# Optimization experiments

Measured on AMD Instinct MI355X. Metric: run time of the kernel, lower is better.

The kernel has to match this reference:

```python
import jax, jax.numpy as jnp
import numpy as np

B, T, P, C = 1, 256, 88, 128   # batch, time frames, 88 piano pitches, hidden_per_pitch
HEADS, WIN, NLAYERS = 4, 25, 2
HD = C // HEADS


def setup_inputs() -> dict:
    ks = jax.random.split(jax.random.key(0), 8)
    s = 0.02
    return {
        "x": jax.random.normal(ks[0], (B, T, P, C), jnp.float32),
        "condition": jax.random.normal(ks[1], (B, T, P, 2), jnp.float32),
        "mask": jax.random.uniform(ks[2], (B, T, P), jnp.float32),
        # fusion linear: Linear(hidden_per_pitch + 3, hidden_per_pitch)
        "linear_w": jax.random.normal(ks[3], (C, C + 3), jnp.float32) * s,
        "linear_b": jnp.zeros((C,), jnp.float32),
        # shared NeighborhoodAttention2D params (nn.Sequential repeats the same module)
        "qkv_w": jax.random.normal(ks[4], (3 * C, C), jnp.float32) * s,
        "qkv_b": jnp.zeros((3 * C,), jnp.float32),
        "rpb": jax.random.normal(ks[5], (HEADS, 2 * WIN - 1, 2 * WIN - 1), jnp.float32) * s,
        "proj_w": jax.random.normal(ks[6], (C, C), jnp.float32) * s,
        "proj_b": jnp.zeros((C,), jnp.float32),
    }


def _nbr_idx(n, w):
    # NATTEN edge-clamped windows: window start is clamped so every query sees w keys.
    start = jnp.clip(jnp.arange(n) - (w - 1) // 2, 0, n - w)
    idx = start[:, None] + jnp.arange(w)             # [n, w] absolute key indices
    rel = idx - jnp.arange(n)[:, None] + (w - 1)     # [n, w] rpb indices in [0, 2w-2]
    return idx, rel


def na2d(x, qkv_w, qkv_b, rpb, proj_w, proj_b):
    b, h, w_, c = x.shape
    qkv = (x @ qkv_w.T + qkv_b).reshape(b, h, w_, 3, HEADS, HD)
    q, k, v = (jnp.moveaxis(qkv[..., i, :, :], 3, 1) for i in range(3))  # [b,heads,h,w,hd]
    q = q * (HD ** -0.5)

    idx_h, rel_h = _nbr_idx(h, WIN)
    idx_w, rel_w = _nbr_idx(w_, WIN)

    def score_step(_, ki):
        kg = k[:, :, idx_h[:, ki]][:, :, :, idx_w]
        s = jnp.einsum('bhijd,bhijkd->bhijk', q, kg)
        s = s + rpb[:, rel_h[:, ki]][:, :, rel_w][None]
        return None, s

    _, scores = jax.lax.scan(score_step, None, jnp.arange(WIN))
    scores = jnp.moveaxis(scores, 0, 4)
    attn = jax.nn.softmax(scores.reshape(b, HEADS, h, w_, WIN * WIN), axis=-1)
    attn = attn.reshape(b, HEADS, h, w_, WIN, WIN)

    def out_step(acc, ki):
        vg = v[:, :, idx_h[:, ki]][:, :, :, idx_w]
        return acc + jnp.einsum('bhijk,bhijkd->bhijd', attn[..., ki, :], vg), None

    out, _ = jax.lax.scan(out_step, jnp.zeros_like(q), jnp.arange(WIN))
    out = jnp.moveaxis(out, 1, 3).reshape(b, h, w_, c)      # merge heads
    return out @ proj_w.T + proj_b


def reference(x, condition, mask, linear_w, linear_b, qkv_w, qkv_b, rpb, proj_w, proj_b):
    cat = jnp.concatenate([x, condition, mask[..., None]], axis=-1)  # [B,T,P,C+3]
    y = jax.nn.relu(cat @ linear_w.T + linear_b)
    for _ in range(NLAYERS):  # same module repeated -> shared weights
        y = na2d(y, qkv_w, qkv_b, rpb, proj_w, proj_b)
    return y
```

## Files before the change

### kernel.cpp

```cpp
#include <hip/hip_runtime.h>
#include <hip/hip_fp16.h>

#define TT 256
#define PP 88
#define CC 128
#define NN (TT * PP)
#define HEADS 4
#define HD 32
#define WIN 25
#define RPBW 49
#define RPBSZ (RPBW * RPBW)
#define SCALE 0.17677669529663687f
#define LOG2E 1.4426950408889634f
#define QSC (SCALE * LOG2E)

#define KVROW 11264
#define KVAARWS 258

#if __has_builtin(__builtin_amdgcn_exp2f)
#define EXP2(x) __builtin_amdgcn_exp2f(x)
#else
#define EXP2(x) exp2f(x)
#endif

typedef _Float16 f16;
typedef f16 f16x8 __attribute__((ext_vector_type(8)));
typedef f16 f16x8u __attribute__((ext_vector_type(8), aligned(4)));
typedef f16 f16x4 __attribute__((ext_vector_type(4)));
typedef f16 f16x4u __attribute__((ext_vector_type(4), aligned(4)));
typedef float f32x4 __attribute__((ext_vector_type(4)));
typedef float f32x4u __attribute__((ext_vector_type(4), aligned(4)));
typedef __fp16 hf16x2 __attribute__((ext_vector_type(2)));
union PkU { hf16x2 h; unsigned u; };


__global__ __launch_bounds__(256) void prep(
    const float* __restrict__ lw, const float* __restrict__ qw,
    const float* __restrict__ pw, const float* __restrict__ qb,
    const float* __restrict__ pb, const float* __restrict__ rpb,
    f16* __restrict__ lwf, f16* __restrict__ qwf, f16* __restrict__ pwf,
    f16* __restrict__ w2f, float* __restrict__ qbs, float* __restrict__ b2s,
    float* __restrict__ rpbp)
{
    const int b = blockIdx.x;
    if (b < 192) {
        int idx = b * 256 + threadIdx.x;
        if (idx < 128 * 160) {
            int r = idx / 160, c = idx - r * 160;
            float v = (c < 131) ? lw[r * 131 + c] : 0.f;
            int lane = (((c & 31) >> 3) << 4) + (r & 15);
            int faddr = (((r >> 6) << 2) + ((r >> 4) & 3)) * 2560 + (c >> 5) * 512 + lane * 8 + (c & 7);
            lwf[faddr] = (f16)v;
        }
        if (idx < 384 * 128) {
            float v = qw[idx];
            if (idx < 128 * 128) v *= QSC;
            int i = idx >> 7, k = idx & 127;
            int lane = (((k & 31) >> 3) << 4) + (i & 15);
            int faddr = (((i >> 6) << 2) + ((i >> 4) & 3)) * 2048 + (k >> 5) * 512 + lane * 8 + (k & 7);
            qwf[faddr] = (f16)v;
        }
        if (idx < 128 * 128) {
            int i = idx >> 7, k = idx & 127;
            int lane = (((k & 31) >> 3) << 4) + (i & 15);
            int faddr = (((i >> 6) << 2) + ((i >> 4) & 3)) * 2048 + (k >> 5) * 512 + lane * 8 + (k & 7);
            pwf[faddr] = (f16)pw[idx];
        }
        if (idx < 384) qbs[idx] = qb[idx] * (idx < 128 ? QSC : 1.f);
        if (idx < 10240) rpbp[idx] = (idx < 4 * RPBSZ) ? rpb[idx] * LOG2E : 0.f;
    } else if (b < 216) {
        int t = (b - 192) * 256 + threadIdx.x;
        int i = t >> 4, l = t & 15;
        if (i < 384) {
            float s = 0.f;
            #pragma unroll
            for (int j = l * 8; j < l * 8 + 8; j++) s += qw[i * 128 + j] * pb[j];
            s += __shfl_xor(s, 1); s += __shfl_xor(s, 2);
            s += __shfl_xor(s, 4); s += __shfl_xor(s, 8);
            if (l == 0) b2s[i] = (qb[i] + s) * (i < 128 ? QSC : 1.f);
        }
    } else {
        const int bw = b - 216;
        const int m0 = (bw & 1) * 64;
        const int n0 = (bw >> 1) * 64;
        const int tid = threadIdx.x;
        const int w = tid >> 6, lane = tid & 63, quad = lane >> 4, nn = lane & 15;
        const int krow = m0 + w * 16 + nn;
        f16x8 af[4];
        #pragma unroll
        for (int ks = 0; ks < 4; ks++) {
            union { f16 e[8]; f16x8 v; } t;
            #pragma unroll
            for (int e = 0; e < 8; e++)
                t.e[e] = (f16)pw[(ks * 32 + quad * 8 + e) * 128 + krow];
            af[ks] = t.v;
        }
        f32x4 acc[4] = {};
        #pragma unroll
        for (int nt = 0; nt < 4; nt++) {
            int irow = n0 + nt * 16 + nn;
            #pragma unroll
            for (int ks = 0; ks < 4; ks++) {
                const float* qr = &qw[(size_t)irow * 128 + ks * 32 + quad * 8];
                float4 a = *(const float4*)qr, bq = *(const float4*)(qr + 4);
                PkU u0, u1, u2, u3;
                u0.h = __builtin_amdgcn_cvt_pkrtz(a.x, a.y);
                u1.h = __builtin_amdgcn_cvt_pkrtz(a.z, a.w);
                u2.h = __builtin_amdgcn_cvt_pkrtz(bq.x, bq.y);
                u3.h = __builtin_amdgcn_cvt_pkrtz(bq.z, bq.w);
                union { unsigned u[4]; f16x8 v; } bb;
                bb.u[0] = u0.u; bb.u[1] = u1.u; bb.u[2] = u2.u; bb.u[3] = u3.u;
                acc[nt] = __builtin_amdgcn_mfma_f32_16x16x32_f16(af[ks], bb.v, acc[nt], 0, 0, 0);
            }
        }
        #pragma unroll
        for (int nt = 0; nt < 4; nt++) {
            int i = n0 + nt * 16 + nn;
            int k = m0 + w * 16 + quad * 4;
            float sc = (i < 128) ? QSC : 1.f;
            PkU p0, p1;
            p0.h = __builtin_amdgcn_cvt_pkrtz(acc[nt][0] * sc, acc[nt][1] * sc);
            p1.h = __builtin_amdgcn_cvt_pkrtz(acc[nt][2] * sc, acc[nt][3] * sc);
            int lane2 = (((k & 31) >> 3) << 4) + (i & 15);
            int faddr = (((i >> 6) << 2) + ((i >> 4) & 3)) * 2048 + (k >> 5) * 512 + lane2 * 8 + (k & 7);
            *(uint2*)&w2f[faddr] = make_uint2(p0.u, p1.u);
        }
    }
}

__global__ __launch_bounds__(256) void fusion_gemm(
    const float* __restrict__ x, const float* __restrict__ cond, const float* __restrict__ mask,
    const f16* __restrict__ lwf, const float* __restrict__ lb, f16* __restrict__ yh)
{
    __shared__ __align__(16) f16 Alds[64 * 168];
    __shared__ __align__(16) f16 Rlds[64][72];
    const int m0 = blockIdx.x * 64, n0 = blockIdx.y * 64;
    const int tid = threadIdx.x;
    const int w = tid >> 6, lane = tid & 63, quad = lane >> 4, nn = lane & 15;

    {
        int r = tid >> 2, cpart = tid & 3;
        size_t pos = m0 + r;
        *(uint4*)&Alds[r * 168 + 128 + cpart * 8] = make_uint4(0, 0, 0, 0);
        const float* xr = x + pos * 128 + cpart * 32;
        #pragma unroll
        for (int t = 0; t < 4; t++) {
            float4 a = *(const float4*)(xr + t * 8);
            float4 b = *(const float4*)(xr + t * 8 + 4);
            PkU p0, p1, p2, p3;
            p0.h = __builtin_amdgcn_cvt_pkrtz(a.x, a.y);
            p1.h = __builtin_amdgcn_cvt_pkrtz(a.z, a.w);
            p2.h = __builtin_amdgcn_cvt_pkrtz(b.x, b.y);
            p3.h = __builtin_amdgcn_cvt_pkrtz(b.z, b.w);
            *(uint4*)&Alds[r * 168 + cpart * 32 + t * 8] = make_uint4(p0.u, p1.u, p2.u, p3.u);
        }
        if (cpart == 0) {
            Alds[r * 168 + 128] = (f16)cond[pos * 2];
            Alds[r * 168 + 129] = (f16)cond[pos * 2 + 1];
            Alds[r * 168 + 130] = (f16)mask[pos];
        }
    }
    __syncthreads();

    const f16* wfb = lwf + ((size_t)(n0 >> 6) * 4 + w) * 2560 + lane * 8;
    f16x8 af[5];
    #pragma unroll
    for (int ks = 0; ks < 5; ks++)
        af[ks] = *(const f16x8*)(wfb + ks * 512);
    f32x4 acc[4] = {};
    #pragma unroll
    for (int ks = 0; ks < 5; ks++)
        #pragma unroll
        for (int nt = 0; nt < 4; nt++) {
            f16x8 bf = *(const f16x8*)&Alds[(nt * 16 + nn) * 168 + ks * 32 + quad * 8];
            acc[nt] = __builtin_amdgcn_mfma_f32_16x16x32_f16(af[ks], bf, acc[nt], 0, 0, 0);
        }
    float bv[4];
    #pragma unroll
    for (int r = 0; r < 4; r++) bv[r] = lb[n0 + w * 16 + quad * 4 + r];
    #pragma unroll
    for (int nt = 0; nt < 4; nt++) {
        PkU p0, p1;
        p0.h = __builtin_amdgcn_cvt_pkrtz(fmaxf(acc[nt][0] + bv[0], 0.f), fmaxf(acc[nt][1] + bv[1], 0.f));
        p1.h = __builtin_amdgcn_cvt_pkrtz(fmaxf(acc[nt][2] + bv[2], 0.f), fmaxf(acc[nt][3] + bv[3], 0.f));
        *(uint2*)&Rlds[nt * 16 + nn][w * 16 + quad * 4] = make_uint2(p0.u, p1.u);
    }
    __syncthreads();
    #pragma unroll
    for (int it = 0; it < 2; it++) {
        int idx = it * 256 + tid;
        int pl = idx >> 3, oct = idx & 7;
        *(uint4*)&yh[(size_t)(m0 + pl) * 128 + n0 + oct * 8] = *(uint4*)&Rlds[pl][oct * 8];
    }
}

__global__ __launch_bounds__(256) void gemm_qkv(
    const f16* __restrict__ A, const f16* __restrict__ Wf, const float* __restrict__ bias,
    f16* __restrict__ qh, f16* __restrict__ kh2, f16* __restrict__ vh2)
{
    __shared__ __align__(16) f16 Alds[64 * 136];
    __shared__ __align__(16) f16 Rlds[64][72];
    const int m0 = blockIdx.x * 64, n0 = blockIdx.y * 64;
    const int tid = threadIdx.x;
    const int w = tid >> 6, lane = tid & 63, quad = lane >> 4, nn = lane & 15;

    for (int i = tid; i < 1024; i += 256) {
        int r = i >> 4, c = i & 15;
        *(uint4*)&Alds[r * 136 + c * 8] = *(const uint4*)&A[(size_t)(m0 + r) * 128 + c * 8];
    }
    __syncthreads();

    const f16* wfb = Wf + ((size_t)(n0 >> 6) * 4 + w) * 2048 + lane * 8;
    f16x8 af[4];
    #pragma unroll
    for (int ks = 0; ks < 4; ks++)
        af[ks] = *(const f16x8*)(wfb + ks * 512);
    f32x4 acc[4] = {};
    #pragma unroll
    for (int ks = 0; ks < 4; ks++)
        #pragma unroll
        for (int nt = 0; nt < 4; nt++) {
            f16x8 bf = *(const f16x8*)&Alds[(nt * 16 + nn) * 136 + ks * 32 + quad * 8];
            acc[nt] = __builtin_amdgcn_mfma_f32_16x16x32_f16(af[ks], bf, acc[nt], 0, 0, 0);
        }
    float bv[4];
    #pragma unroll
    for (int r = 0; r < 4; r++) bv[r] = bias[n0 + w * 16 + quad * 4 + r];

    if (n0 < 256) {
        #pragma unroll
        for (int nt = 0; nt < 4; nt++) {
            PkU p0, p1;
            p0.h = __builtin_amdgcn_cvt_pkrtz(acc[nt][0] + bv[0], acc[nt][1] + bv[1]);
            p1.h = __builtin_amdgcn_cvt_pkrtz(acc[nt][2] + bv[2], acc[nt][3] + bv[3]);
            *(uint2*)&Rlds[nt * 16 + nn][w * 16 + quad * 4] = make_uint2(p0.u, p1.u);
        }
    } else {
        #pragma unroll
        for (int nt = 0; nt < 4; nt++) {
            union { f16 e[4]; uint2 u; } t;
            #pragma unroll
            for (int r = 0; r < 4; r++) t.e[r] = (f16)(acc[nt][r] + bv[r]);
            *(uint2*)&Rlds[nt * 16 + nn][w * 16 + quad * 4] = t.u;
        }
    }
    __syncthreads();

    if (n0 < 128) {
        #pragma unroll
        for (int it = 0; it < 2; it++) {
            int idx = it * 256 + tid;
            int pl = idx >> 3, oct = idx & 7;
            f16x8 v = *(const f16x8*)&Rlds[pl][oct * 8];
            *(uint4*)&qh[(size_t)(m0 + pl) * 128 + n0 + oct * 8] = *(uint4*)&v;
        }
    } else if (n0 < 256) {
        #pragma unroll
        for (int it = 0; it < 2; it++) {
            int idx = it * 256 + tid;
            int pl = idx >> 3, oct = idx & 7;
            f16x8 v = *(const f16x8*)&Rlds[pl][oct * 8];
            int pos = m0 + pl, aa = pos / 88, j = pos - aa * 88;
            int ch = n0 - 128 + oct * 8;
            int h = ch >> 5, c32 = ch & 31;
            *(uint4*)&kh2[((size_t)(aa * 4 + h) * 88 + j) * 32 + c32] = *(uint4*)&v;
        }
    } else {
        #pragma unroll
        for (int it = 0; it < 2; it++) {
            int idx = it * 256 + tid;
            int pq = idx >> 5, cp = idx & 31;
            union { f16 e[8]; uint4 u; } t;
            #pragma unroll
            for (int cc = 0; cc < 2; cc++)
                #pragma unroll
                for (int jj = 0; jj < 4; jj++)
                    t.e[cc * 4 + jj] = Rlds[pq * 4 + jj][cp * 2 + cc];
            int pos = m0 + pq * 4, aa = pos / 88, j = pos - aa * 88;
            int ch = n0 - 256 + cp * 2;
            int h = ch >> 5, c = ch & 31, half = c >> 4, c16 = c & 15;
            *(uint4*)&vh2[(size_t)(aa * 4 + h) * 2816 + half * 1408 + (j >> 2) * 64 + c16 * 4] = t.u;
        }
    }
}

__global__ __launch_bounds__(256) void gemm_out(
    const f16* __restrict__ A, const f16* __restrict__ Wf, const float* __restrict__ bias,
    float* __restrict__ outp)
{
    __shared__ __align__(16) f16 Alds[64 * 136];
    __shared__ __align__(16) float Rldsf[64][68];
    const int m0 = blockIdx.x * 64, n0 = blockIdx.y * 64;
    const int tid = threadIdx.x;
    const int w = tid >> 6, lane = tid & 63, quad = lane >> 4, nn = lane & 15;

    for (int i = tid; i < 1024; i += 256) {
        int r = i >> 4, c = i & 15;
        *(uint4*)&Alds[r * 136 + c * 8] = *(const uint4*)&A[(size_t)(m0 + r) * 128 + c * 8];
    }
    __syncthreads();

    const f16* wfb = Wf + ((size_t)(n0 >> 6) * 4 + w) * 2048 + lane * 8;
    f16x8 af[4];
    #pragma unroll
    for (int ks = 0; ks < 4; ks++)
        af[ks] = *(const f16x8*)(wfb + ks * 512);
    f32x4 acc[4] = {};
    #pragma unroll
    for (int ks = 0; ks < 4; ks++)
        #pragma unroll
        for (int nt = 0; nt < 4; nt++) {
            f16x8 bf = *(const f16x8*)&Alds[(nt * 16 + nn) * 136 + ks * 32 + quad * 8];
            acc[nt] = __builtin_amdgcn_mfma_f32_16x16x32_f16(af[ks], bf, acc[nt], 0, 0, 0);
        }
    float bv[4];
    #pragma unroll
    for (int r = 0; r < 4; r++) bv[r] = bias[n0 + w * 16 + quad * 4 + r];
    #pragma unroll
    for (int nt = 0; nt < 4; nt++) {
        f32x4 vv;
        #pragma unroll
        for (int r = 0; r < 4; r++) vv[r] = acc[nt][r] + bv[r];
        *(f32x4*)&Rldsf[nt * 16 + nn][w * 16 + quad * 4] = vv;
    }
    __syncthreads();
    #pragma unroll
    for (int it = 0; it < 4; it++) {
        int idx = it * 256 + tid;
        int pl = idx >> 4, part = idx & 15;
        *(f32x4*)&outp[(size_t)(m0 + pl) * 128 + n0 + part * 4] = *(const f32x4*)&Rldsf[pl][part * 4];
    }
}

__global__ __launch_bounds__(256, 3) void attn_mfma(
    const f16* __restrict__ qh,
    const f16* __restrict__ kh2,
    const f16* __restrict__ vh2,
    const float* __restrict__ rpbp,
    f16* __restrict__ ao)
{
    const int bx = ((blockIdx.x & 7) << 3) + (blockIdx.x >> 3);
    const int i0 = bx * 4;
    const int j0 = blockIdx.y * 8;
    const int tid = threadIdx.x;
    const int w = tid >> 6, lane = tid & 63;
    const int quad = lane >> 4, nn = lane & 15;
    const int kh = w & 1;
    const int hs = w >> 1;
    const int h  = blockIdx.z * 2 + hs;

    const int ri0 = min(max(i0 - 12, 0), TT - 28);
    const int rj0 = min(max(j0 - 12, 0), PP - WIN) & ~3;

    __shared__ __align__(16) float Olds[2][64][28];

    int si_[2];
    unsigned pm_[2][4];
    f16x8 qf[2];
    const float* rpq[2];
    const float* rp_h = rpbp + h * RPBSZ;
    const int aa0 = ri0 + kh * 14;

    #pragma unroll
    for (int q = 0; q < 2; q++) {
        int ql = q * 16 + nn;
        int qi = i0 + (ql >> 3), qj = j0 + (ql & 7);
        int si = min(max(qi - 12, 0), TT - WIN);
        int sj = min(max(qj - 12, 0), PP - WIN);
        si_[q] = si;
        unsigned cm = 0x1FFFFFFu << (sj - rj0);
        #pragma unroll
        for (int t = 0; t < 4; t++) {
            int k0 = (t >> 1) * 16 + quad * 4 + (t & 1) * 2;
            pm_[q][t] = (((cm >> k0) & 1u) ? 0xFFFFu : 0u)
                      | (((cm >> (k0 + 1)) & 1u) ? 0xFFFF0000u : 0u);
        }
        qf[q] = *(const f16x8*)&qh[(size_t)(qi * PP + qj) * 128 + h * HD + quad * 8];
        rpq[q] = rp_h + (aa0 - qi + 24) * RPBW + (rj0 - qj + 24) + quad * 4;
    }

    const int b0 = min(rj0 + nn, PP - 1);
    const int b1 = min(rj0 + 16 + nn, PP - 1);
    const f16x4 ones4 = {(f16)1.f, (f16)1.f, (f16)1.f, (f16)1.f};

    const f16* kb = kh2 + (size_t)(aa0 * 4 + h) * 2816 + quad * 8;
    const f16* vb = vh2 + (size_t)(aa0 * 4 + h) * 2816 + ((rj0 >> 2) + quad) * 64 + nn * 4;

    f32x4 O[2][2] = {};
    f32x4 lacc[2] = {};
    union PB { unsigned u[2]; f16x4 v; };
    PB pa_[2], pb_[2];
    f32x4 za_[2], zb_[2];

    int aa = aa0;
    f16x8 kf0 = *(const f16x8*)(kb + (size_t)b0 * 32);
    f16x8 kf1 = *(const f16x8*)(kb + (size_t)b1 * 32);
    f16x4 vfA0 = *(const f16x4u*)vb;
    f16x4 vfB0 = *(const f16x4u*)(vb + 256);
    f16x4 vfA1 = *(const f16x4u*)(vb + 1408);
    f16x4 vfB1 = *(const f16x4u*)(vb + 1664);
    #pragma unroll
    for (int q = 0; q < 2; q++) {
        za_[q] = *(const f32x4u*)rpq[q];
        zb_[q] = *(const f32x4u*)(rpq[q] + 16);
        rpq[q] += RPBW;
    }
    #pragma unroll
    for (int q = 0; q < 2; q++) {
        f32x4 s0 = __builtin_amdgcn_mfma_f32_16x16x32_f16(kf0, qf[q], za_[q], 0, 0, 0);
        f32x4 s1 = __builtin_amdgcn_mfma_f32_16x16x32_f16(kf1, qf[q], zb_[q], 0, 0, 0);
        bool rv = (unsigned)(aa - si_[q]) <= 24u;
        float p[8];
        #pragma unroll
        for (int r = 0; r < 4; r++) { p[r] = EXP2(s0[r]); p[r + 4] = EXP2(s1[r]); }
        PkU u0, u1, u2, u3;
        u0.h = __builtin_amdgcn_cvt_pkrtz(p[0], p[1]);
        u1.h = __builtin_amdgcn_cvt_pkrtz(p[2], p[3]);
        u2.h = __builtin_amdgcn_cvt_pkrtz(p[4], p[5]);
        u3.h = __builtin_amdgcn_cvt_pkrtz(p[6], p[7]);
        pa_[q].u[0] = rv ? (u0.u & pm_[q][0]) : 0u;
        pa_[q].u[1] = rv ? (u1.u & pm_[q][1]) : 0u;
        pb_[q].u[0] = rv ? (u2.u & pm_[q][2]) : 0u;
        pb_[q].u[1] = rv ? (u3.u & pm_[q][3]) : 0u;
    }
    kb += KVROW;
    f16x8 nkf0 = *(const f16x8*)(kb + (size_t)b0 * 32);
    f16x8 nkf1 = *(const f16x8*)(kb + (size_t)b1 * 32);

    #pragma unroll
    for (int c = 1; c < 14; ++c) {
        aa = aa0 + c;
        kf0 = nkf0; kf1 = nkf1;

        #pragma unroll
        for (int q = 0; q < 2; q++) {
            za_[q] = *(const f32x4u*)rpq[q];
            zb_[q] = *(const f32x4u*)(rpq[q] + 16);
            rpq[q] += RPBW;
        }

        __builtin_amdgcn_s_setprio(1);
        #pragma unroll
        for (int q = 0; q < 2; q++) {
            O[q][0] = __builtin_amdgcn_mfma_f32_16x16x16f16(pa_[q].v, vfA0, O[q][0], 0, 0, 0);
            O[q][0] = __builtin_amdgcn_mfma_f32_16x16x16f16(pb_[q].v, vfB0, O[q][0], 0, 0, 0);
            O[q][1] = __builtin_amdgcn_mfma_f32_16x16x16f16(pa_[q].v, vfA1, O[q][1], 0, 0, 0);
            O[q][1] = __builtin_amdgcn_mfma_f32_16x16x16f16(pb_[q].v, vfB1, O[q][1], 0, 0, 0);
            lacc[q] = __builtin_amdgcn_mfma_f32_16x16x16f16(pa_[q].v, ones4, lacc[q], 0, 0, 0);
            lacc[q] = __builtin_amdgcn_mfma_f32_16x16x16f16(pb_[q].v, ones4, lacc[q], 0, 0, 0);
        }
        __builtin_amdgcn_s_setprio(0);

        vb += KVROW;
        vfA0 = *(const f16x4u*)vb;
        vfB0 = *(const f16x4u*)(vb + 256);
        vfA1 = *(const f16x4u*)(vb + 1408);
        vfB1 = *(const f16x4u*)(vb + 1664);

        kb += KVROW;
        nkf0 = *(const f16x8*)(kb + (size_t)b0 * 32);
        nkf1 = *(const f16x8*)(kb + (size_t)b1 * 32);

        #pragma unroll
        for (int q = 0; q < 2; q++) {
            f32x4 s0 = __builtin_amdgcn_mfma_f32_16x16x32_f16(kf0, qf[q], za_[q], 0, 0, 0);
            f32x4 s1 = __builtin_amdgcn_mfma_f32_16x16x32_f16(kf1, qf[q], zb_[q], 0, 0, 0);
            bool rv = (unsigned)(aa - si_[q]) <= 24u;
            float p[8];
            #pragma unroll
            for (int r = 0; r < 4; r++) { p[r] = EXP2(s0[r]); p[r + 4] = EXP2(s1[r]); }
            PkU u0, u1, u2, u3;
            u0.h = __builtin_amdgcn_cvt_pkrtz(p[0], p[1]);
            u1.h = __builtin_amdgcn_cvt_pkrtz(p[2], p[3]);
            u2.h = __builtin_amdgcn_cvt_pkrtz(p[4], p[5]);
            u3.h = __builtin_amdgcn_cvt_pkrtz(p[6], p[7]);
            pa_[q].u[0] = rv ? (u0.u & pm_[q][0]) : 0u;
            pa_[q].u[1] = rv ? (u1.u & pm_[q][1]) : 0u;
            pb_[q].u[0] = rv ? (u2.u & pm_[q][2]) : 0u;
            pb_[q].u[1] = rv ? (u3.u & pm_[q][3]) : 0u;
        }
    }

    #pragma unroll
    for (int q = 0; q < 2; q++) {
        O[q][0] = __builtin_amdgcn_mfma_f32_16x16x16f16(pa_[q].v, vfA0, O[q][0], 0, 0, 0);
        O[q][0] = __builtin_amdgcn_mfma_f32_16x16x16f16(pb_[q].v, vfB0, O[q][0], 0, 0, 0);
        O[q][1] = __builtin_amdgcn_mfma_f32_16x16x16f16(pa_[q].v, vfA1, O[q][1], 0, 0, 0);
        O[q][1] = __builtin_amdgcn_mfma_f32_16x16x16f16(pb_[q].v, vfB1, O[q][1], 0, 0, 0);
        lacc[q] = __builtin_amdgcn_mfma_f32_16x16x16f16(pa_[q].v, ones4, lacc[q], 0, 0, 0);
        lacc[q] = __builtin_amdgcn_mfma_f32_16x16x16f16(pb_[q].v, ones4, lacc[q], 0, 0, 0);
    }

    if (kh) {
        float* ob = &Olds[hs][lane][0];
        #pragma unroll
        for (int q = 0; q < 2; q++) {
            *(f32x4*)&ob[q * 12]     = O[q][0];
            *(f32x4*)&ob[q * 12 + 4] = O[q][1];
            *(f32x4*)&ob[q * 12 + 8] = lacc[q];
        }
    }
    __syncthreads();
    if (!kh) {
        const float* ob = &Olds[hs][lane][0];
        #pragma unroll
        for (int q = 0; q < 2; q++) {
            f32x4 o0 = O[q][0] + *(const f32x4*)&ob[q * 12];
            f32x4 o1 = O[q][1] + *(const f32x4*)&ob[q * 12 + 4];
            f32x4 la = lacc[q] + *(const f32x4*)&ob[q * 12 + 8];
            #pragma unroll
            for (int r = 0; r < 4; r++) {
                float li = 1.f / la[r];
                int ql = q * 16 + quad * 4 + r;
                int qi = i0 + (ql >> 3), qj = j0 + (ql & 7);
                size_t base = (size_t)(qi * PP + qj) * CC + h * HD;
                ao[base + nn]      = (f16)(o0[r] * li);
                ao[base + 16 + nn] = (f16)(o1[r] * li);
            }
        }
    }
}

extern "C" void kernel_launch(void* const* d_in, const int* in_sizes, int n_in,
                              void* d_out, int out_size, void* d_ws, size_t ws_size,
                              hipStream_t stream) {
    (void)in_sizes; (void)n_in; (void)out_size; (void)ws_size;
    const float* x    = (const float*)d_in[0];
    const float* cond = (const float*)d_in[1];
    const float* mask = (const float*)d_in[2];
    const float* lw   = (const float*)d_in[3];
    const float* lb   = (const float*)d_in[4];
    const float* qw   = (const float*)d_in[5];
    const float* qb   = (const float*)d_in[6];
    const float* rpb  = (const float*)d_in[7];
    const float* pw   = (const float*)d_in[8];
    const float* pb   = (const float*)d_in[9];
    float* outp       = (float*)d_out;

    float* ws   = (float*)d_ws;
    float* qbs  = ws;
    float* b2s  = qbs + 384;
    float* rpbp = b2s + 384;
    f16* lwf  = (f16*)(rpbp + 10240);
    f16* qwf  = lwf + 20480;
    f16* pwf  = qwf + 49152;
    f16* w2f  = pwf + 16384;
    f16* yh   = w2f + 49152;
    f16* qh   = yh + (size_t)NN * 128;
    f16* kh2  = qh + (size_t)NN * 128;
    f16* vh2  = kh2 + (size_t)KVAARWS * KVROW;
    f16* ao   = vh2 + (size_t)KVAARWS * KVROW;

    prep<<<228, 256, 0, stream>>>(lw, qw, pw, qb, pb, rpb, lwf, qwf, pwf, w2f, qbs, b2s, rpbp);
    fusion_gemm<<<dim3(352, 2), 256, 0, stream>>>(x, cond, mask, lwf, lb, yh);
    gemm_qkv<<<dim3(352, 6), 256, 0, stream>>>(yh, qwf, qbs, qh, kh2, vh2);
    attn_mfma<<<dim3(TT / 4, PP / 8, HEADS / 2), 256, 0, stream>>>(qh, kh2, vh2, rpbp, ao);
    gemm_qkv<<<dim3(352, 6), 256, 0, stream>>>(ao, w2f, b2s, qh, kh2, vh2);
    attn_mfma<<<dim3(TT / 4, PP / 8, HEADS / 2), 256, 0, stream>>>(qh, kh2, vh2, rpbp, ao);
    gemm_out<<<dim3(352, 2), 256, 0, stream>>>(ao, pwf, pb, outp);
}
```

Baseline: 181.5 us.

## Fuse input fusion GEMM with first QKV projection; vectorize weight prep

Merges the fusion linear+ReLU kernel with the first QKV GEMM so each 64-row block computes y in LDS and then loops over all six QKV output tiles. This removes the yh round-trip through global memory and one kernel launch. The cost is a 352-block grid, down from 704 and 2112 blocks, which lowers parallelism on the device. Weight repacking in prep is also rewritten to write 8 halves per thread with vector stores, replacing scattered scalar stores.

```diff
diff --git a/kernel.cpp b/kernel.cpp
--- a/kernel.cpp
+++ b/kernel.cpp
@@ -45,29 +45,48 @@
     const int b = blockIdx.x;
     if (b < 192) {
         int idx = b * 256 + threadIdx.x;
-        if (idx < 128 * 160) {
-            int r = idx / 160, c = idx - r * 160;
-            float v = (c < 131) ? lw[r * 131 + c] : 0.f;
-            int lane = (((c & 31) >> 3) << 4) + (r & 15);
-            int faddr = (((r >> 6) << 2) + ((r >> 4) & 3)) * 2560 + (c >> 5) * 512 + lane * 8 + (c & 7);
-            lwf[faddr] = (f16)v;
-        }
-        if (idx < 384 * 128) {
-            float v = qw[idx];
-            if (idx < 128 * 128) v *= QSC;
-            int i = idx >> 7, k = idx & 127;
-            int lane = (((k & 31) >> 3) << 4) + (i & 15);
-            int faddr = (((i >> 6) << 2) + ((i >> 4) & 3)) * 2048 + (k >> 5) * 512 + lane * 8 + (k & 7);
-            qwf[faddr] = (f16)v;
-        }
-        if (idx < 128 * 128) {
-            int i = idx >> 7, k = idx & 127;
-            int lane = (((k & 31) >> 3) << 4) + (i & 15);
-            int faddr = (((i >> 6) << 2) + ((i >> 4) & 3)) * 2048 + (k >> 5) * 512 + lane * 8 + (k & 7);
-            pwf[faddr] = (f16)pw[idx];
-        }
-        if (idx < 384) qbs[idx] = qb[idx] * (idx < 128 ? QSC : 1.f);
-        if (idx < 10240) rpbp[idx] = (idx < 4 * RPBSZ) ? rpb[idx] * LOG2E : 0.f;
+        if (idx < 6144) {
+            int group = idx >> 8, ks = (idx >> 6) & 3, lane = idx & 63;
+            int i = (group >> 2) * 64 + (group & 3) * 16 + (lane & 15);
+            int k0 = ks * 32 + (lane >> 4) * 8;
+            float sc = (i < 128) ? QSC : 1.f;
+            union { f16 e[8]; uint4 u; } t;
+            #pragma unroll
+            for (int e = 0; e < 8; e++) t.e[e] = (f16)(qw[i * 128 + k0 + e] * sc);
+            *(uint4*)&qwf[group * 2048 + ks * 512 + lane * 8] = t.u;
+        } else if (idx < 8704) {
+            int j = idx - 6144;
+            int group = j >> 8, rem = j & 255;
+            if (j < 2560) { }
+            int ks = rem >> 6, lane = rem & 63;
+            group = j / 320; int r2 = j - group * 320; ks = r2 >> 6; lane = r2 & 63;
+            if (group < 8) {
+                int r = (group >> 2) * 64 + (group & 3) * 16 + (lane & 15);
+                int c0 = ks * 32 + (lane >> 4) * 8;
+                union { f16 e[8]; uint4 u; } t;
+                #pragma unroll
+                for (int e = 0; e < 8; e++) {
+                    int c = c0 + e;
+                    t.e[e] = (f16)((c < 131) ? lw[r * 131 + c] : 0.f);
+                }
+                *(uint4*)&lwf[group * 2560 + ks * 512 + lane * 8] = t.u;
+            }
+        } else if (idx < 10752) {
+            int j = idx - 8704;
+            int group = j >> 8, ks = (j >> 6) & 3, lane = j & 63;
+            int i = (group >> 2) * 64 + (group & 3) * 16 + (lane & 15);
+            int k0 = ks * 32 + (lane >> 4) * 8;
+            union { f16 e[8]; uint4 u; } t;
+            #pragma unroll
+            for (int e = 0; e < 8; e++) t.e[e] = (f16)pw[i * 128 + k0 + e];
+            *(uint4*)&pwf[group * 2048 + ks * 512 + lane * 8] = t.u;
+        } else if (idx < 20992) {
+            int j = idx - 10752;
+            rpbp[j] = (j < 4 * RPBSZ) ? rpb[j] * LOG2E : 0.f;
+        } else if (idx < 21376) {
+            int j = idx - 20992;
+            qbs[j] = qb[j] * (j < 128 ? QSC : 1.f);
+        }
     } else if (b < 216) {
         int t = (b - 192) * 256 + threadIdx.x;
         int i = t >> 4, l = t & 15;
@@ -128,13 +147,16 @@
     }
 }
 
-__global__ __launch_bounds__(256) void fusion_gemm(
+__global__ __launch_bounds__(256) void fused_fusion_qkv(
     const float* __restrict__ x, const float* __restrict__ cond, const float* __restrict__ mask,
-    const f16* __restrict__ lwf, const float* __restrict__ lb, f16* __restrict__ yh)
+    const f16* __restrict__ lwf, const float* __restrict__ lb,
+    const f16* __restrict__ qwf, const float* __restrict__ bias,
+    f16* __restrict__ qh, f16* __restrict__ kh2, f16* __restrict__ vh2)
 {
     __shared__ __align__(16) f16 Alds[64 * 168];
+    __shared__ __align__(16) f16 Ylds[64 * 136];
     __shared__ __align__(16) f16 Rlds[64][72];
-    const int m0 = blockIdx.x * 64, n0 = blockIdx.y * 64;
+    const int m0 = blockIdx.x * 64;
     const int tid = threadIdx.x;
     const int w = tid >> 6, lane = tid & 63, quad = lane >> 4, nn = lane & 15;
 
@@ -162,35 +184,111 @@
     }
     __syncthreads();
 
-    const f16* wfb = lwf + ((size_t)(n0 >> 6) * 4 + w) * 2560 + lane * 8;
-    f16x8 af[5];
-    #pragma unroll
-    for (int ks = 0; ks < 5; ks++)
-        af[ks] = *(const f16x8*)(wfb + ks * 512);
-    f32x4 acc[4] = {};
-    #pragma unroll
-    for (int ks = 0; ks < 5; ks++)
+    #pragma unroll
+    for (int gi = 0; gi < 2; gi++) {
+        const int g = gi * 4 + w;
+        const int cb = gi * 64 + w * 16;
+        const f16* wfb = lwf + (size_t)g * 2560 + lane * 8;
+        f16x8 af[5];
+        #pragma unroll
+        for (int ks = 0; ks < 5; ks++)
+            af[ks] = *(const f16x8*)(wfb + ks * 512);
+        f32x4 acc[4] = {};
+        #pragma unroll
+        for (int ks = 0; ks < 5; ks++)
+            #pragma unroll
+            for (int nt = 0; nt < 4; nt++) {
+                f16x8 bf = *(const f16x8*)&Alds[(nt * 16 + nn) * 168 + ks * 32 + quad * 8];
+                acc[nt] = __builtin_amdgcn_mfma_f32_16x16x32_f16(af[ks], bf, acc[nt], 0, 0, 0);
+            }
+        float bv[4];
+        #pragma unroll
+        for (int r = 0; r < 4; r++) bv[r] = lb[cb + quad * 4 + r];
         #pragma unroll
         for (int nt = 0; nt < 4; nt++) {
-            f16x8 bf = *(const f16x8*)&Alds[(nt * 16 + nn) * 168 + ks * 32 + quad * 8];
-            acc[nt] = __builtin_amdgcn_mfma_f32_16x16x32_f16(af[ks], bf, acc[nt], 0, 0, 0);
-        }
-    float bv[4];
-    #pragma unroll
-    for (int r = 0; r < 4; r++) bv[r] = lb[n0 + w * 16 + quad * 4 + r];
-    #pragma unroll
-    for (int nt = 0; nt < 4; nt++) {
-        PkU p0, p1;
-        p0.h = __builtin_amdgcn_cvt_pkrtz(fmaxf(acc[nt][0] + bv[0], 0.f), fmaxf(acc[nt][1] + bv[1], 0.f));
-        p1.h = __builtin_amdgcn_cvt_pkrtz(fmaxf(acc[nt][2] + bv[2], 0.f), fmaxf(acc[nt][3] + bv[3], 0.f));
-        *(uint2*)&Rlds[nt * 16 + nn][w * 16 + quad * 4] = make_uint2(p0.u, p1.u);
+            PkU p0, p1;
+            p0.h = __builtin_amdgcn_cvt_pkrtz(fmaxf(acc[nt][0] + bv[0], 0.f), fmaxf(acc[nt][1] + bv[1], 0.f));
+            p1.h = __builtin_amdgcn_cvt_pkrtz(fmaxf(acc[nt][2] + bv[2], 0.f), fmaxf(acc[nt][3] + bv[3], 0.f));
+            *(uint2*)&Ylds[(nt * 16 + nn) * 136 + cb + quad * 4] = make_uint2(p0.u, p1.u);
+        }
     }
     __syncthreads();
-    #pragma unroll
-    for (int it = 0; it < 2; it++) {
-        int idx = it * 256 + tid;
-        int pl = idx >> 3, oct = idx & 7;
-        *(uint4*)&yh[(size_t)(m0 + pl) * 128 + n0 + oct * 8] = *(uint4*)&Rlds[pl][oct * 8];
+
+    #pragma unroll 1
+    for (int t = 0; t < 6; t++) {
+        const int n0 = t * 64;
+        const f16* wfb = qwf + ((size_t)t * 4 + w) * 2048 + lane * 8;
+        f16x8 af[4];
+        #pragma unroll
+        for (int ks = 0; ks < 4; ks++)
+            af[ks] = *(const f16x8*)(wfb + ks * 512);
+        f32x4 acc[4] = {};
+        #pragma unroll
+        for (int ks = 0; ks < 4; ks++)
+            #pragma unroll
+            for (int nt = 0; nt < 4; nt++) {
+                f16x8 bf = *(const f16x8*)&Ylds[(nt * 16 + nn) * 136 + ks * 32 + quad * 8];
+                acc[nt] = __builtin_amdgcn_mfma_f32_16x16x32_f16(af[ks], bf, acc[nt], 0, 0, 0);
+            }
+        float bv[4];
+        #pragma unroll
+        for (int r = 0; r < 4; r++) bv[r] = bias[n0 + w * 16 + quad * 4 + r];
+
+        __syncthreads();
+        if (n0 < 256) {
+            #pragma unroll
+            for (int nt = 0; nt < 4; nt++) {
+                PkU p0, p1;
+                p0.h = __builtin_amdgcn_cvt_pkrtz(acc[nt][0] + bv[0], acc[nt][1] + bv[1]);
+                p1.h = __builtin_amdgcn_cvt_pkrtz(acc[nt][2] + bv[2], acc[nt][3] + bv[3]);
+                *(uint2*)&Rlds[nt * 16 + nn][w * 16 + quad * 4] = make_uint2(p0.u, p1.u);
+            }
+        } else {
+            #pragma unroll
+            for (int nt = 0; nt < 4; nt++) {
+                union { f16 e[4]; uint2 u; } tt;
+                #pragma unroll
+                for (int r = 0; r < 4; r++) tt.e[r] = (f16)(acc[nt][r] + bv[r]);
+                *(uint2*)&Rlds[nt * 16 + nn][w * 16 + quad * 4] = tt.u;
+            }
+        }
+        __syncthreads();
+
+        if (n0 < 128) {
+            #pragma unroll
+            for (int it = 0; it < 2; it++) {
+                int idx = it * 256 + tid;
+                int pl = idx >> 3, oct = idx & 7;
+                *(uint4*)&qh[(size_t)(m0 + pl) * 128 + n0 + oct * 8] = *(uint4*)&Rlds[pl][oct * 8];
+            }
+        } else if (n0 < 256) {
+            #pragma unroll
+            for (int it = 0; it < 2; it++) {
+                int idx = it * 256 + tid;
+                int pl = idx >> 3, oct = idx & 7;
+                f16x8 v = *(const f16x8*)&Rlds[pl][oct * 8];
+                int pos = m0 + pl, aa = pos / 88, j = pos - aa * 88;
+                int ch = n0 - 128 + oct * 8;
+                int h = ch >> 5, c32 = ch & 31;
+                *(uint4*)&kh2[((size_t)(aa * 4 + h) * 88 + j) * 32 + c32] = *(uint4*)&v;
+            }
+        } else {
+            #pragma unroll
+            for (int it = 0; it < 2; it++) {
+                int idx = it * 256 + tid;
+                int pq = idx >> 5, cp = idx & 31;
+                union { f16 e[8]; uint4 u; } tt;
+                #pragma unroll
+                for (int cc = 0; cc < 2; cc++)
+                    #pragma unroll
+                    for (int jj = 0; jj < 4; jj++)
+                        tt.e[cc * 4 + jj] = Rlds[pq * 4 + jj][cp * 2 + cc];
+                int pos = m0 + pq * 4, aa = pos / 88, j = pos - aa * 88;
+                int ch = n0 - 256 + cp * 2;
+                int h = ch >> 5, c = ch & 31, half = c >> 4, c16 = c & 15;
+                *(uint4*)&vh2[(size_t)(aa * 4 + h) * 2816 + half * 1408 + (j >> 2) * 64 + c16 * 4] = tt.u;
+            }
+        }
     }
 }
 
@@ -552,8 +650,7 @@
     f16* ao   = vh2 + (size_t)KVAARWS * KVROW;
 
     prep<<<228, 256, 0, stream>>>(lw, qw, pw, qb, pb, rpb, lwf, qwf, pwf, w2f, qbs, b2s, rpbp);
-    fusion_gemm<<<dim3(352, 2), 256, 0, stream>>>(x, cond, mask, lwf, lb, yh);
-    gemm_qkv<<<dim3(352, 6), 256, 0, stream>>>(yh, qwf, qbs, qh, kh2, vh2);
+    fused_fusion_qkv<<<352, 256, 0, stream>>>(x, cond, mask, lwf, lb, qwf, qbs, qh, kh2, vh2);
     attn_mfma<<<dim3(TT / 4, PP / 8, HEADS / 2), 256, 0, stream>>>(qh, kh2, vh2, rpbp, ao);
     gemm_qkv<<<dim3(352, 6), 256, 0, stream>>>(ao, w2f, b2s, qh, kh2, vh2);
     attn_mfma<<<dim3(TT / 4, PP / 8, HEADS / 2), 256, 0, stream>>>(qh, kh2, vh2, rpbp, ao);
```

New measurement: 180.8 us. No clear change (-0.4%).
